# Kernel tuning notes

Measured on AMD Instinct MI355X. Metric: run time of the kernel, lower is better.

Reference implementation:

```python
import jax, jax.numpy as jnp
import numpy as np
from jax import lax

WS = (4, 8, 8)        # window_size (D,H,W)
DIM = 128
HEADS = 4
HD = DIM // HEADS      # 32
SCALE = HD ** -0.5     # swinv1, lif neuron -> head_dim**-0.5
TAU = 2.0
VTH = 1.0
ALPHA = 2.0            # ATan surrogate width


def _rel_pos_index(ws):
    # static numpy computation of relative_position_index, shape (N, N)
    coords = np.stack(np.meshgrid(np.arange(ws[0]), np.arange(ws[1]), np.arange(ws[2]), indexing='ij'))
    cf = coords.reshape(3, -1)                      # (3, N)
    rel = (cf[:, :, None] - cf[:, None, :]).transpose(1, 2, 0).astype(np.int64)  # (N,N,3)
    rel[:, :, 0] += ws[0] - 1
    rel[:, :, 1] += ws[1] - 1
    rel[:, :, 2] += ws[2] - 1
    rel[:, :, 0] *= (2 * ws[1] - 1) * (2 * ws[2] - 1)
    rel[:, :, 1] *= 2 * ws[2] - 1
    return rel.sum(-1)

RPI = _rel_pos_index(WS)  # (N, N) int


@jax.custom_vjp
def spike(x):
    return (x >= 0.0).astype(x.dtype)

def _spike_fwd(x):
    return spike(x), x

def _spike_bwd(x, g):
    # ATan surrogate gradient (spikingjelly default)
    return (g * (ALPHA / (2.0 * (1.0 + (np.pi / 2.0 * ALPHA * x) ** 2))),)

spike.defvjp(_spike_fwd, _spike_bwd)


def lif(x):
    # multi-step LIF over leading time axis: v' = v + (x - v)/tau, hard reset to 0
    def step(v, xt):
        v = v + (xt - v) / TAU
        s = spike(v - VTH)
        return v * (1.0 - s), s
    return lax.scan(step, jnp.zeros_like(x[0]), x)[1]


def setup_inputs() -> dict:
    key = jax.random.key(0)
    ks = jax.random.split(key, 7)
    x = jax.random.normal(ks[0], (WS[0], 256, WS[1], WS[2], DIM), dtype=jnp.float32)
    Wq = jax.random.normal(ks[1], (DIM, DIM), dtype=jnp.float32) * 0.02
    Wk = jax.random.normal(ks[2], (DIM, DIM), dtype=jnp.float32) * 0.02
    Wv = jax.random.normal(ks[3], (DIM, DIM), dtype=jnp.float32) * 0.02
    rpb_table = jax.random.normal(ks[4], ((2 * WS[0] - 1) * (2 * WS[1] - 1) * (2 * WS[2] - 1), HEADS), dtype=jnp.float32) * 0.02
    Wproj = jax.random.normal(ks[5], (DIM, DIM), dtype=jnp.float32) * 0.02
    bproj = jax.random.normal(ks[6], (DIM,), dtype=jnp.float32) * 0.02
    return {"x": x, "Wq": Wq, "Wk": Wk, "Wv": Wv, "rpb_table": rpb_table, "Wproj": Wproj, "bproj": bproj}


def reference(x, Wq, Wk, Wv, rpb_table, Wproj, bproj):
    T, B_, H, W, C = x.shape
    N = T * H * W
    # QKV: linear (no bias) -> spiking neuron over time axis
    q = lif(jnp.einsum('tbhwc,dc->tbhwd', x, Wq))
    k = lif(jnp.einsum('tbhwc,dc->tbhwd', x, Wk))
    v = lif(jnp.einsum('tbhwc,dc->tbhwd', x, Wv))
    # literal row-major reshape as in torch: (T,B_,H,W,C) -> (B_, heads, N, hd)
    q = q.reshape(B_, HEADS, N, HD)
    k = k.reshape(B_, HEADS, N, HD)
    v = v.reshape(B_, HEADS, N, HD)
    # scaled QK^T (NO softmax in the original forward)
    attn = jnp.einsum('bhnd,bhmd->bhnm', q * SCALE, k)
    rpb = rpb_table[RPI.reshape(-1)].reshape(N, N, HEADS).transpose(2, 0, 1)  # (heads,N,N)
    attn = attn + rpb[None]
    out = jnp.einsum('bhnm,bhmd->bhnd', attn, v)
    out = out.reshape(B_, HEADS, T, H, W, HD).transpose(2, 0, 3, 4, 1, 5).reshape(T, B_, H, W, C)
    out = jnp.einsum('tbhwc,dc->tbhwd', out, Wproj) + bproj
    out = lif(out).reshape(B_, N, C)
    return (out, attn)
```

## Files before the change

### kernel.cpp

```cpp
#include <hip/hip_runtime.h>
#include <hip/hip_bf16.h>


typedef __attribute__((ext_vector_type(8))) short bf16x8;
typedef __attribute__((ext_vector_type(4))) float f32x4;

#define MFMA16(a, b, c) __builtin_amdgcn_mfma_f32_16x16x32_bf16((a), (b), (c), 0, 0, 0)

__device__ __forceinline__ unsigned short f2bf(float f) {
    union { __hip_bfloat16 h; unsigned short u; } cv;
    cv.h = __float2bfloat16(f);
    return cv.u;
}

__device__ __forceinline__ void cvt8_store(unsigned short* dst, const float* src) {
    float4 f0 = *(const float4*)(src);
    float4 f1 = *(const float4*)(src + 4);
    unsigned short h[8];
    h[0] = f2bf(f0.x); h[1] = f2bf(f0.y); h[2] = f2bf(f0.z); h[3] = f2bf(f0.w);
    h[4] = f2bf(f1.x); h[5] = f2bf(f1.y); h[6] = f2bf(f1.z); h[7] = f2bf(f1.w);
    *(uint4*)dst = *(const uint4*)h;
}

__global__ __launch_bounds__(256) void k_rpb_expand(
    const float* __restrict__ tbl, float* __restrict__ rpbx)
{
    int idx = blockIdx.x * 256 + threadIdx.x;
    int hh = idx >> 16;
    int n = (idx >> 8) & 255, m = idx & 255;
    int zn = n >> 6, yn = (n >> 3) & 7, xn = n & 7;
    int zm = m >> 6, ym = (m >> 3) & 7, xm = m & 7;
    int ri = (zn - zm + 3) * 225 + (yn - ym + 7) * 15 + (xn - xm + 7);
    rpbx[idx] = tbl[ri * 4 + hh];
}

__global__ __launch_bounds__(256) void k_qkv_lif(
    const float* __restrict__ x,
    const float* __restrict__ Wq,
    const float* __restrict__ Wk,
    const float* __restrict__ Wv,
    unsigned int* __restrict__ qbits,
    unsigned int* __restrict__ kbits,
    unsigned int* __restrict__ vbits)
{
    __shared__ unsigned short Wl[128 * 136];
    __shared__ unsigned short Xl[64 * 136];

    const int tid = threadIdx.x;
    const int wv = tid >> 6, lane = tid & 63;
    const int l15 = lane & 15, lh = lane >> 4;
    const int wsel = blockIdx.y;
    const float* W = (wsel == 0) ? Wq : (wsel == 1) ? Wk : Wv;
    unsigned int* bits = (wsel == 0) ? qbits : (wsel == 1) ? kbits : vbits;
    const int B = blockIdx.x;

    {
#pragma unroll
        for (int i = 0; i < 8; ++i) {
            int e = i * 2048 + tid * 8;
            int r = e >> 7, cc = e & 127;
            cvt8_store(&Wl[r * 136 + cc], W + r * 128 + cc);
        }
    }

    f32x4 vst[8];
#pragma unroll
    for (int nt = 0; nt < 8; ++nt) vst[nt] = (f32x4){0.f, 0.f, 0.f, 0.f};

    for (int t = 0; t < 4; ++t) {
        __syncthreads();
        const float* xg = x + t * 2097152 + B * 8192;
#pragma unroll
        for (int i = 0; i < 4; ++i) {
            int e = i * 2048 + tid * 8;
            int r = e >> 7, cc = e & 127;
            cvt8_store(&Xl[r * 136 + cc], xg + r * 128 + cc);
        }
        __syncthreads();

        f32x4 acc[8];
#pragma unroll
        for (int nt = 0; nt < 8; ++nt) acc[nt] = (f32x4){0.f, 0.f, 0.f, 0.f};
#pragma unroll
        for (int kk = 0; kk < 4; ++kk) {
            bf16x8 a = *(const bf16x8*)&Xl[(wv * 16 + l15) * 136 + kk * 32 + lh * 8];
#pragma unroll
            for (int nt = 0; nt < 8; ++nt) {
                bf16x8 b = *(const bf16x8*)&Wl[(nt * 16 + l15) * 136 + kk * 32 + lh * 8];
                acc[nt] = MFMA16(a, b, acc[nt]);
            }
        }
        unsigned short sp[8][4];
#pragma unroll
        for (int nt = 0; nt < 8; ++nt) {
#pragma unroll
            for (int reg = 0; reg < 4; ++reg) {
                float y = acc[nt][reg];
                float v = vst[nt][reg];
                v = v + (y - v) * 0.5f;
                float s = (v >= 1.0f) ? 1.0f : 0.0f;
                vst[nt][reg] = v * (1.0f - s);
                sp[nt][reg] = (s != 0.0f) ? (unsigned short)1 : (unsigned short)0;
            }
        }
        __syncthreads();
#pragma unroll
        for (int nt = 0; nt < 8; ++nt)
#pragma unroll
            for (int reg = 0; reg < 4; ++reg)
                Xl[(wv * 16 + lh * 4 + reg) * 136 + nt * 16 + l15] = sp[nt][reg];
        __syncthreads();
        {
            const unsigned short* rowp = &Xl[(tid >> 2) * 136 + (tid & 3) * 32];
            unsigned int mask = 0;
#pragma unroll
            for (int j8 = 0; j8 < 4; ++j8) {
                uint4 u = *(const uint4*)(rowp + j8 * 8);
                int base = j8 * 8;
                if (u.x & 0xFFFFu) mask |= 1u << (base + 0);
                if (u.x >> 16)     mask |= 1u << (base + 1);
                if (u.y & 0xFFFFu) mask |= 1u << (base + 2);
                if (u.y >> 16)     mask |= 1u << (base + 3);
                if (u.z & 0xFFFFu) mask |= 1u << (base + 4);
                if (u.z >> 16)     mask |= 1u << (base + 5);
                if (u.w & 0xFFFFu) mask |= 1u << (base + 6);
                if (u.w >> 16)     mask |= 1u << (base + 7);
            }
            bits[(t * 256 + B) * 256 + tid] = mask;
        }
    }
}

__global__ __launch_bounds__(256) void k_attn(
    const unsigned int* __restrict__ qbits,
    const unsigned int* __restrict__ kbits,
    const unsigned int* __restrict__ vbits,
    const float* __restrict__ rpbx,
    float* __restrict__ attn_out,
    unsigned short* __restrict__ o_ws)
{
    __shared__ unsigned int  qb[256];
    __shared__ unsigned short vT[32 * 264];
    __shared__ unsigned short attnL[64 * 264];

    const int tid = threadIdx.x;
    const int wv = tid >> 6, lane = tid & 63;
    const int l15 = lane & 15, lh = lane >> 4;
    const int g = blockIdx.x, hh = g & 3;

    qb[tid] = qbits[g * 256 + tid];
    uint4 km = *(const uint4*)&kbits[g * 256 + (tid & 63) * 4];
    {
        unsigned int vb = vbits[g * 256 + tid];
#pragma unroll
        for (int d = 0; d < 32; ++d)
            vT[d * 264 + tid] = ((vb >> d) & 1u) ? (unsigned short)0x3F80
                                                 : (unsigned short)0;
    }
    __syncthreads();

    const float SC = 0.17677669529663687f;
    float* attn_b = attn_out + (size_t)g * 65536;
    const float* rp = rpbx + hh * 65536;
    unsigned short* ob = o_ws + g * 8192;
    const int rg = tid >> 6, m0 = (tid & 63) * 4;

    for (int c = 0; c < 4; ++c) {
#pragma unroll
        for (int j = 0; j < 16; ++j) {
            int n = c * 64 + j * 4 + rg;
            unsigned int qn = qb[n];
            float4 rp4 = *(const float4*)&rp[n * 256 + m0];
            f32x4 av;
            av.x = (float)__popc(qn & km.x) * SC + rp4.x;
            av.y = (float)__popc(qn & km.y) * SC + rp4.y;
            av.z = (float)__popc(qn & km.z) * SC + rp4.z;
            av.w = (float)__popc(qn & km.w) * SC + rp4.w;
            __builtin_nontemporal_store(av, (f32x4*)(attn_b + n * 256 + m0));
            unsigned int p0 = (unsigned int)f2bf(av.x) | ((unsigned int)f2bf(av.y) << 16);
            unsigned int p1 = (unsigned int)f2bf(av.z) | ((unsigned int)f2bf(av.w) << 16);
            uint2 pk; pk.x = p0; pk.y = p1;
            *(uint2*)&attnL[(j * 4 + rg) * 264 + m0] = pk;
        }
        __syncthreads();
        f32x4 oc[2];
        oc[0] = (f32x4){0.f, 0.f, 0.f, 0.f};
        oc[1] = (f32x4){0.f, 0.f, 0.f, 0.f};
#pragma unroll
        for (int kk = 0; kk < 8; ++kk) {
            bf16x8 a = *(const bf16x8*)&attnL[(wv * 16 + l15) * 264 + kk * 32 + lh * 8];
#pragma unroll
            for (int nt = 0; nt < 2; ++nt) {
                bf16x8 b = *(const bf16x8*)&vT[(nt * 16 + l15) * 264 + kk * 32 + lh * 8];
                oc[nt] = MFMA16(a, b, oc[nt]);
            }
        }
#pragma unroll
        for (int nt = 0; nt < 2; ++nt) {
#pragma unroll
            for (int reg = 0; reg < 4; ++reg) {
                int n = c * 64 + wv * 16 + lh * 4 + reg;
                ob[n * 32 + nt * 16 + l15] = f2bf(oc[nt][reg]);
            }
        }
        __syncthreads();
    }
}

__global__ __launch_bounds__(256) void k_proj_lif(
    const unsigned short* __restrict__ o_ws,
    const float* __restrict__ Wp,
    const float* __restrict__ bp,
    float* __restrict__ out0)
{
    __shared__ unsigned short Wl[128 * 136];
    __shared__ unsigned short Al[64 * 136];

    const int tid = threadIdx.x;
    const int wv = tid >> 6, lane = tid & 63;
    const int l15 = lane & 15, lh = lane >> 4;
    const int b = blockIdx.x;

    {
#pragma unroll
        for (int i = 0; i < 8; ++i) {
            int e = i * 2048 + tid * 8;
            int r = e >> 7, cc = e & 127;
            cvt8_store(&Wl[r * 136 + cc], Wp + r * 128 + cc);
        }
    }

    float biasf[2];
#pragma unroll
    for (int ntl = 0; ntl < 2; ++ntl)
        biasf[ntl] = bp[(wv * 2 + ntl) * 16 + l15];

    const unsigned short* ob = o_ws + b * 32768;

    for (int c = 0; c < 4; ++c) {
        __syncthreads();
#pragma unroll
        for (int i = 0; i < 4; ++i) {
            int e = i * 2048 + tid * 8;
            int lr2 = e >> 7, cc = e & 127;
            int t2 = lr2 >> 4, rit = lr2 & 15;
            int hhh = cc >> 5, hd = cc & 31;
            int n = t2 * 64 + c * 16 + rit;
            *(uint4*)&Al[lr2 * 136 + cc] =
                *(const uint4*)(ob + (hhh * 256 + n) * 32 + hd);
        }
        __syncthreads();

        f32x4 acc[4][2];
#pragma unroll
        for (int t2 = 0; t2 < 4; ++t2)
#pragma unroll
            for (int ntl = 0; ntl < 2; ++ntl)
                acc[t2][ntl] = (f32x4){0.f, 0.f, 0.f, 0.f};
#pragma unroll
        for (int kk = 0; kk < 4; ++kk) {
            bf16x8 a[4];
#pragma unroll
            for (int t2 = 0; t2 < 4; ++t2)
                a[t2] = *(const bf16x8*)&Al[(t2 * 16 + l15) * 136 + kk * 32 + lh * 8];
#pragma unroll
            for (int ntl = 0; ntl < 2; ++ntl) {
                bf16x8 bb = *(const bf16x8*)&Wl[((wv * 2 + ntl) * 16 + l15) * 136 + kk * 32 + lh * 8];
#pragma unroll
                for (int t2 = 0; t2 < 4; ++t2)
                    acc[t2][ntl] = MFMA16(a[t2], bb, acc[t2][ntl]);
            }
        }
#pragma unroll
        for (int ntl = 0; ntl < 2; ++ntl) {
            int d = (wv * 2 + ntl) * 16 + l15;
#pragma unroll
            for (int reg = 0; reg < 4; ++reg) {
                int hw = c * 16 + lh * 4 + reg;
                float v = 0.f;
#pragma unroll
                for (int t2 = 0; t2 < 4; ++t2) {
                    float y = acc[t2][ntl][reg] + biasf[ntl];
                    v = v + (y - v) * 0.5f;
                    float s = (v >= 1.0f) ? 1.0f : 0.0f;
                    v = v * (1.0f - s);
                    out0[t2 * 2097152 + b * 8192 + hw * 128 + d] = s;
                }
            }
        }
    }
}

extern "C" void kernel_launch(void* const* d_in, const int* in_sizes, int n_in,
                              void* d_out, int out_size, void* d_ws, size_t ws_size,
                              hipStream_t stream)
{
    const float* x   = (const float*)d_in[0];
    const float* Wq  = (const float*)d_in[1];
    const float* Wk  = (const float*)d_in[2];
    const float* Wv  = (const float*)d_in[3];
    const float* tbl = (const float*)d_in[4];
    const float* Wp  = (const float*)d_in[5];
    const float* bp  = (const float*)d_in[6];

    float* out0 = (float*)d_out;
    float* attn = out0 + 8388608;

    unsigned short* o_ws = (unsigned short*)d_ws;
    unsigned int* qbits = (unsigned int*)(o_ws + 8388608);
    unsigned int* kbits = qbits + 262144;
    unsigned int* vbits = kbits + 262144;
    float* rpbx = (float*)(vbits + 262144);

    k_rpb_expand<<<1024, 256, 0, stream>>>(tbl, rpbx);
    k_qkv_lif<<<dim3(256, 3), 256, 0, stream>>>(x, Wq, Wk, Wv, qbits, kbits, vbits);
    k_attn<<<1024, 256, 0, stream>>>(qbits, kbits, vbits, rpbx, attn, o_ws);
    k_proj_lif<<<256, 256, 0, stream>>>(o_ws, Wp, bp, out0);
}
```

Measured before the change: 354.3 us.

## Fuse RPB expansion into QKV kernel and shrink attention chunk to 32 rows

Drops the separate relative-position-bias expansion kernel and runs it as an extra blockIdx.y slice of the QKV+LIF launch, now writing float4 per thread. That removes one kernel launch and lets the expansion overlap with the QKV work. The attention kernel now processes 32-row chunks instead of 64, which halves the attnL shared buffer and splits the MFMA work across waves as row-tile × head-dim-half. The projection output now uses nontemporal stores. The smaller chunks mean twice as many barriers per block, in exchange for less LDS use and possibly higher occupancy.

```diff
diff --git a/kernel.cpp b/kernel.cpp
--- a/kernel.cpp
+++ b/kernel.cpp
@@ -22,27 +22,34 @@
     *(uint4*)dst = *(const uint4*)h;
 }
 
-__global__ __launch_bounds__(256) void k_rpb_expand(
-    const float* __restrict__ tbl, float* __restrict__ rpbx)
-{
-    int idx = blockIdx.x * 256 + threadIdx.x;
-    int hh = idx >> 16;
-    int n = (idx >> 8) & 255, m = idx & 255;
-    int zn = n >> 6, yn = (n >> 3) & 7, xn = n & 7;
-    int zm = m >> 6, ym = (m >> 3) & 7, xm = m & 7;
-    int ri = (zn - zm + 3) * 225 + (yn - ym + 7) * 15 + (xn - xm + 7);
-    rpbx[idx] = tbl[ri * 4 + hh];
-}
-
 __global__ __launch_bounds__(256) void k_qkv_lif(
     const float* __restrict__ x,
     const float* __restrict__ Wq,
     const float* __restrict__ Wk,
     const float* __restrict__ Wv,
+    const float* __restrict__ tbl,
     unsigned int* __restrict__ qbits,
     unsigned int* __restrict__ kbits,
-    unsigned int* __restrict__ vbits)
+    unsigned int* __restrict__ vbits,
+    float* __restrict__ rpbx)
 {
+    if (blockIdx.y == 3) {
+        int base = blockIdx.x * 1024 + threadIdx.x * 4;
+        int hh = base >> 16;
+        int n = (base >> 8) & 255, m0 = base & 255;
+        int zn = n >> 6, yn = (n >> 3) & 7, xn = n & 7;
+        float4 o;
+#pragma unroll
+        for (int i = 0; i < 4; ++i) {
+            int m = m0 + i;
+            int zm = m >> 6, ym = (m >> 3) & 7, xm = m & 7;
+            int ri = (zn - zm + 3) * 225 + (yn - ym + 7) * 15 + (xn - xm + 7);
+            ((float*)&o)[i] = tbl[ri * 4 + hh];
+        }
+        *(float4*)&rpbx[base] = o;
+        return;
+    }
+
     __shared__ unsigned short Wl[128 * 136];
     __shared__ unsigned short Xl[64 * 136];
 
@@ -141,7 +148,7 @@
 {
     __shared__ unsigned int  qb[256];
     __shared__ unsigned short vT[32 * 264];
-    __shared__ unsigned short attnL[64 * 264];
+    __shared__ unsigned short attnL[32 * 264];
 
     const int tid = threadIdx.x;
     const int wv = tid >> 6, lane = tid & 63;
@@ -163,12 +170,13 @@
     float* attn_b = attn_out + (size_t)g * 65536;
     const float* rp = rpbx + hh * 65536;
     unsigned short* ob = o_ws + g * 8192;
-    const int rg = tid >> 6, m0 = (tid & 63) * 4;
-
-    for (int c = 0; c < 4; ++c) {
-#pragma unroll
-        for (int j = 0; j < 16; ++j) {
-            int n = c * 64 + j * 4 + rg;
+    const int rg = wv, m0 = (tid & 63) * 4;
+    const int rt = wv >> 1, nh = wv & 1;
+
+    for (int c = 0; c < 8; ++c) {
+#pragma unroll
+        for (int j = 0; j < 8; ++j) {
+            int n = c * 32 + j * 4 + rg;
             unsigned int qn = qb[n];
             float4 rp4 = *(const float4*)&rp[n * 256 + m0];
             f32x4 av;
@@ -183,25 +191,17 @@
             *(uint2*)&attnL[(j * 4 + rg) * 264 + m0] = pk;
         }
         __syncthreads();
-        f32x4 oc[2];
-        oc[0] = (f32x4){0.f, 0.f, 0.f, 0.f};
-        oc[1] = (f32x4){0.f, 0.f, 0.f, 0.f};
+        f32x4 oc = (f32x4){0.f, 0.f, 0.f, 0.f};
 #pragma unroll
         for (int kk = 0; kk < 8; ++kk) {
-            bf16x8 a = *(const bf16x8*)&attnL[(wv * 16 + l15) * 264 + kk * 32 + lh * 8];
-#pragma unroll
-            for (int nt = 0; nt < 2; ++nt) {
-                bf16x8 b = *(const bf16x8*)&vT[(nt * 16 + l15) * 264 + kk * 32 + lh * 8];
-                oc[nt] = MFMA16(a, b, oc[nt]);
-            }
-        }
-#pragma unroll
-        for (int nt = 0; nt < 2; ++nt) {
-#pragma unroll
-            for (int reg = 0; reg < 4; ++reg) {
-                int n = c * 64 + wv * 16 + lh * 4 + reg;
-                ob[n * 32 + nt * 16 + l15] = f2bf(oc[nt][reg]);
-            }
+            bf16x8 a = *(const bf16x8*)&attnL[(rt * 16 + l15) * 264 + kk * 32 + lh * 8];
+            bf16x8 b = *(const bf16x8*)&vT[(nh * 16 + l15) * 264 + kk * 32 + lh * 8];
+            oc = MFMA16(a, b, oc);
+        }
+#pragma unroll
+        for (int reg = 0; reg < 4; ++reg) {
+            int n = c * 32 + rt * 16 + lh * 4 + reg;
+            ob[n * 32 + nh * 16 + l15] = f2bf(oc[reg]);
         }
         __syncthreads();
     }
@@ -284,7 +284,8 @@
                     v = v + (y - v) * 0.5f;
                     float s = (v >= 1.0f) ? 1.0f : 0.0f;
                     v = v * (1.0f - s);
-                    out0[t2 * 2097152 + b * 8192 + hw * 128 + d] = s;
+                    __builtin_nontemporal_store(
+                        s, out0 + t2 * 2097152 + b * 8192 + hw * 128 + d);
                 }
             }
         }
@@ -312,8 +313,8 @@
     unsigned int* vbits = kbits + 262144;
     float* rpbx = (float*)(vbits + 262144);
 
-    k_rpb_expand<<<1024, 256, 0, stream>>>(tbl, rpbx);
-    k_qkv_lif<<<dim3(256, 3), 256, 0, stream>>>(x, Wq, Wk, Wv, qbits, kbits, vbits);
+    k_qkv_lif<<<dim3(256, 4), 256, 0, stream>>>(x, Wq, Wk, Wv, tbl,
+                                                qbits, kbits, vbits, rpbx);
     k_attn<<<1024, 256, 0, stream>>>(qbits, kbits, vbits, rpbx, attn, o_ws);
     k_proj_lif<<<256, 256, 0, stream>>>(o_ws, Wp, bp, out0);
 }
```

Result: no change. 352.7 us (-0.5%).
